# Kernel optimization log

Measured on AMD Instinct MI355X. Metric: run time of the kernel, lower is better.

Reference implementation:

```python
import jax, jax.numpy as jnp
import numpy as np

B, S, E = 4, 2048, 1024
H = 4
DH = E // H          # 256 head dim
DQ = E // 4          # 256 quaternion d_model
ALPHA = 1.5
EPS = 1e-10
FOCUS = 0.9
SEL = 2.0


def setup_inputs() -> dict:
    key = jax.random.key(0)
    ks = jax.random.split(key, 6)
    sc = 0.02
    return {
        "x": jax.random.normal(ks[0], (B, S, E), dtype=jnp.float32),
        "in_proj_w": jax.random.normal(ks[1], (3 * E, E), dtype=jnp.float32) * sc,
        "in_proj_b": jnp.zeros((3 * E,), dtype=jnp.float32),
        "out_w": jax.random.normal(ks[2], (E, E), dtype=jnp.float32) * sc,
        "out_b": jnp.zeros((E,), dtype=jnp.float32),
        "m_w1": jax.random.normal(ks[3], (E, E), dtype=jnp.float32) * sc,
        "m_b1": jnp.zeros((E,), dtype=jnp.float32),
        "m_w2": jax.random.normal(ks[4], (E, E), dtype=jnp.float32) * sc,
        "m_b2": jnp.zeros((E,), dtype=jnp.float32),
    }


def quaternion_multiply(q1, q2):
    # Hamilton product over last dim of size 4 (complex-valued components).
    w1, x1, y1, z1 = q1[..., 0], q1[..., 1], q1[..., 2], q1[..., 3]
    w2, x2, y2, z2 = q2[..., 0], q2[..., 1], q2[..., 2], q2[..., 3]
    return jnp.stack([
        w1 * w2 - x1 * x2 - y1 * y2 - z1 * z2,
        w1 * x2 + x1 * w2 + y1 * z2 - z1 * y2,
        w1 * y2 - x1 * z2 + y1 * w2 + z1 * x2,
        w1 * z2 + x1 * y2 - y1 * x2 + z1 * w2,
    ], axis=-1)


def _mha(x, in_proj_w, in_proj_b, out_w, out_b):
    # torch nn.MultiheadAttention self-attention, batch_first
    qkv = x @ in_proj_w.T + in_proj_b              # [B,S,3E]
    q, k, v = jnp.split(qkv, 3, axis=-1)
    q = q.reshape(B, S, H, DH)
    k = k.reshape(B, S, H, DH)
    v = v.reshape(B, S, H, DH)
    scores = jnp.einsum('bqhd,bkhd->bhqk', q, k) / jnp.sqrt(jnp.float32(DH))
    attn = jax.nn.softmax(scores, axis=-1)
    out = jnp.einsum('bhqk,bkhd->bqhd', attn, v).reshape(B, S, E)
    return out @ out_w.T + out_b


def _spectral_attention(signal):
    sq = signal.reshape(B, S, DQ, 4)
    sfft = jnp.fft.fft(sq, axis=-3)                 # complex64, FFT over seq
    kk = jnp.arange(S, dtype=jnp.float32)
    filt = jnp.exp(1j * ALPHA * jnp.arctan(jnp.log(kk + EPS)))  # [S] complex
    sf = sfft * filt[None, :, None, None]
    inter = quaternion_multiply(quaternion_multiply(sf, sf), sf)
    attended = jnp.fft.ifft(inter, axis=-3).real
    return attended.reshape(B, S, E)


def reference(x, in_proj_w, in_proj_b, out_w, out_b, m_w1, m_b1, m_w2, m_b2):
    nicotinic = _mha(x, in_proj_w, in_proj_b, out_w, out_b)
    h = jax.nn.gelu(x @ m_w1.T + m_b1, approximate=False)
    muscarinic = h @ m_w2.T + m_b2
    chol = FOCUS * nicotinic + (1.0 - FOCUS) * muscarinic
    attn_w = _spectral_attention(chol * SEL)
    return x * attn_w
```

## Files before the change

### kernel.cpp

```cpp
#include <hip/hip_runtime.h>
#include <cstdint>

typedef _Float16 f16;
typedef unsigned short u16;
typedef __attribute__((ext_vector_type(8))) _Float16 half8;
typedef __attribute__((ext_vector_type(2))) __fp16 fp16x2;
typedef __attribute__((ext_vector_type(4))) float f32x4;

#define MFMA_F16(a, b, c) __builtin_amdgcn_mfma_f32_16x16x32_f16(a, b, c, 0, 0, 0)

#define WAITVM8() asm volatile("s_waitcnt vmcnt(8)" ::: "memory")
#define WAITVM4() asm volatile("s_waitcnt vmcnt(4)" ::: "memory")
#define WAITVM0() asm volatile("s_waitcnt vmcnt(0)" ::: "memory")
#define BARRIER() do { asm volatile("" ::: "memory"); __builtin_amdgcn_s_barrier(); \
                       asm volatile("" ::: "memory"); } while (0)

__device__ inline void stage16(const void* g, void* l) {
#if defined(__has_builtin) && __has_builtin(__builtin_amdgcn_global_load_lds)
  __builtin_amdgcn_global_load_lds(
      (const __attribute__((address_space(1))) unsigned*)g,
      (__attribute__((address_space(3))) unsigned*)l, 16, 0, 0);
#else
  *(int4*)l = *(const int4*)g;
#endif
}

__device__ inline int pack_f16(float a, float b) {
#if defined(__has_builtin) && __has_builtin(__builtin_amdgcn_cvt_pkrtz)
  union { fp16x2 h; int i; } u;
  u.h = __builtin_amdgcn_cvt_pkrtz(a, b);
  return u.i;
#else
  union { f16 h[2]; int i; } u;
  u.h[0] = (f16)a; u.h[1] = (f16)b;
  return u.i;
#endif
}

__global__ __launch_bounds__(256)
void conv_all(const float* __restrict__ x, const float* __restrict__ wqkv,
              const float* __restrict__ w1, const float* __restrict__ wout,
              const float* __restrict__ w2, f16* __restrict__ dst) {
  int i = (blockIdx.x * 256 + threadIdx.x) * 8;
  const float* src; size_t dofs; float sc = 1.0f;
  if (i < 8388608)       { src = x + i;               dofs = i; }
  else if (i < 11534336) { src = wqkv + (i - 8388608); dofs = i; }
  else if (i < 12582912) { src = w1 + (i - 11534336);  dofs = i; }
  else if (i < 13631488) {
    int t = i - 12582912; int j = t >> 10, k = t & 1023;
    src = wout + t; dofs = 12582912 + (size_t)j * 2048 + k; sc = 1.8f;
  } else {
    int t = i - 13631488; int j = t >> 10, k = t & 1023;
    src = w2 + t; dofs = 12582912 + (size_t)j * 2048 + 1024 + k; sc = 0.2f;
  }
  float4 a = *(const float4*)src;
  float4 b = *(const float4*)(src + 4);
  half8 h;
  h[0] = (f16)(a.x * sc); h[1] = (f16)(a.y * sc); h[2] = (f16)(a.z * sc); h[3] = (f16)(a.w * sc);
  h[4] = (f16)(b.x * sc); h[5] = (f16)(b.y * sc); h[6] = (f16)(b.z * sc); h[7] = (f16)(b.w * sc);
  *(half8*)(dst + dofs) = h;
}

template<int EPI>
__global__ __launch_bounds__(256, 2)
void gemm_f16(const f16* __restrict__ A, const f16* __restrict__ W,
              const float* __restrict__ bias0, const float* __restrict__ bias1,
              void* __restrict__ out0, void* __restrict__ out1, int N, int K) {
  __shared__ __align__(16) f16 lds[2][16384];
  const int tid = threadIdx.x;
  const int lane = tid & 63, w = tid >> 6;
  const int g = lane >> 4, lm = lane & 15;
  const int wr = w >> 1, wc = w & 1;
  const int m0 = blockIdx.y * 128, n0 = blockIdx.x * 128;

  const f16* src[8];
#pragma unroll
  for (int j = 0; j < 8; ++j) {
    int u = j * 256 + tid;
    if (u < 1024) {
      int row = u >> 3, s = u & 7;
      src[j] = A + (size_t)(m0 + row) * K + ((s ^ (row & 7)) << 3);
    } else {
      int v = u - 1024;
      int row = v >> 3, s = v & 7;
      src[j] = W + (size_t)(n0 + row) * K + ((s ^ (row & 7)) << 3);
    }
  }

  f32x4 acc[4][4];
#pragma unroll
  for (int mt = 0; mt < 4; ++mt)
#pragma unroll
    for (int nt = 0; nt < 4; ++nt) acc[mt][nt] = (f32x4){0.f, 0.f, 0.f, 0.f};

#pragma unroll
  for (int j = 0; j < 8; ++j) stage16(src[j], &lds[0][(j * 256 + tid) * 8]);
  __syncthreads();

  const int KT = K >> 6;
#pragma unroll 1
  for (int t = 0; t < KT; ++t) {
    const f16* bufA = lds[t & 1];
    const f16* bufB = bufA + 8192;
    if (t + 1 < KT) {
#pragma unroll
      for (int j = 0; j < 8; ++j) {
        src[j] += 64;
        stage16(src[j], &lds[(t + 1) & 1][(j * 256 + tid) * 8]);
      }
      WAITVM8();
    } else {
      WAITVM0();
    }
    BARRIER();
#pragma unroll
    for (int ks = 0; ks < 2; ++ks) {
      half8 a[4], b[4];
#pragma unroll
      for (int mt = 0; mt < 4; ++mt) {
        int row = wr * 64 + mt * 16 + lm;
        a[mt] = *(const half8*)(bufA + row * 64 + (((ks * 4 + g) ^ (row & 7)) << 3));
      }
#pragma unroll
      for (int nt = 0; nt < 4; ++nt) {
        int row = wc * 64 + nt * 16 + lm;
        b[nt] = *(const half8*)(bufB + row * 64 + (((ks * 4 + g) ^ (row & 7)) << 3));
      }
#pragma unroll
      for (int mt = 0; mt < 4; ++mt)
#pragma unroll
        for (int nt = 0; nt < 4; ++nt)
          acc[mt][nt] = MFMA_F16(a[mt], b[nt], acc[mt][nt]);
    }
    BARRIER();
  }

  const int crow = m0 + wr * 64 + g * 4;
  const int ccol = n0 + wc * 64 + lm;
  if (EPI == 3) {
    if (n0 < 3072) {
      f16* qk = (f16*)out0;
#pragma unroll
      for (int nt = 0; nt < 4; ++nt) {
        float bb = bias0[ccol + nt * 16];
#pragma unroll
        for (int mt = 0; mt < 4; ++mt)
#pragma unroll
          for (int r = 0; r < 4; ++r)
            qk[(size_t)(crow + mt * 16 + r) * 3072 + ccol + nt * 16] =
                (f16)(acc[mt][nt][r] + bb);
      }
    } else {
      f16* cat = (f16*)out1;
      const int hc = ccol - 3072;
#pragma unroll
      for (int nt = 0; nt < 4; ++nt) {
        float bb = bias1[hc + nt * 16];
#pragma unroll
        for (int mt = 0; mt < 4; ++mt)
#pragma unroll
          for (int r = 0; r < 4; ++r) {
            float v = acc[mt][nt][r] + bb;
            v = 0.5f * v * (1.0f + erff(v * 0.70710678118654752f));
            cat[(size_t)(crow + mt * 16 + r) * 2048 + 1024 + hc + nt * 16] = (f16)v;
          }
      }
    }
  } else {
    float* ch = (float*)out0;
#pragma unroll
    for (int nt = 0; nt < 4; ++nt) {
      float bb = 1.8f * bias0[ccol + nt * 16] + 0.2f * bias1[ccol + nt * 16];
#pragma unroll
      for (int mt = 0; mt < 4; ++mt)
#pragma unroll
        for (int r = 0; r < 4; ++r)
          ch[(size_t)(crow + mt * 16 + r) * 1024 + ccol + nt * 16] =
              acc[mt][nt][r] + bb;
    }
  }
}

__global__ __launch_bounds__(256)
void vtrans(const f16* __restrict__ qkv, f16* __restrict__ Vt) {
  __shared__ unsigned vlds[64][65];
  const int tid = threadIdx.x;
  const int bh = blockIdx.x >> 5, st = blockIdx.x & 31;
  const int b = bh >> 2, h = bh & 3;
  const int s0 = st * 64;
  const u16* q16 = (const u16*)qkv;
  u16* v16 = (u16*)Vt;
#pragma unroll 1
  for (int dc = 0; dc < 4; ++dc) {
    __syncthreads();
#pragma unroll 1
    for (int i = 0; i < 16; ++i) {
      int idx = i * 256 + tid;
      int s = idx >> 6, dl = idx & 63;
      vlds[dl][s] = q16[(size_t)(b * 2048 + s0 + s) * 3072 + 2048 + h * 256 + dc * 64 + dl];
    }
    __syncthreads();
#pragma unroll 1
    for (int i = 0; i < 16; ++i) {
      int idx = i * 256 + tid;
      int dl = idx >> 6, s = idx & 63;
      v16[((size_t)bh * 256 + dc * 64 + dl) * 2048 + s0 + s] = (u16)vlds[dl][s];
    }
  }
}

__global__ __launch_bounds__(256, 2)
void flash_f16(const f16* __restrict__ qkv, const f16* __restrict__ Vt,
               f16* __restrict__ attn) {
  __shared__ __align__(16) f16 lds[32768];
  const int tid = threadIdx.x;
  const int lane = tid & 63, w = tid >> 6;
  const int g = lane >> 4, lm = lane & 15;
  const int raw = blockIdx.x;
  const int bh = (raw & 7) * 2 + (raw >> 8);
  const int qt = (raw >> 3) & 31;
  const int b = bh >> 2, h = bh & 3;
  const int q0 = qt * 64 + w * 16;
  const float SC = 0.09016844005555896f;

  half8 qf[8];
  {
    const f16* qp = qkv + (size_t)(b * 2048 + q0 + lm) * 3072 + h * 256 + g * 8;
#pragma unroll
    for (int c = 0; c < 8; ++c) qf[c] = *(const half8*)(qp + c * 32);
  }

  const f16* kbase = qkv + (size_t)b * 2048 * 3072 + 1024 + h * 256;
  const f16* vbase = Vt + (size_t)bh * 256 * 2048;
  int kofs[4], vofs[4];
#pragma unroll
  for (int j = 0; j < 4; ++j) {
    int u = j * 256 + tid;
    int kv = u >> 5, s = u & 31;
    kofs[j] = kv * 3072 + ((s ^ (kv & 7)) << 3);
    int d = u >> 2, sl = u & 3;
    vofs[j] = d * 2048 + ((sl ^ ((d >> 1) & 3)) << 3);
  }

  f32x4 o[16];
#pragma unroll
  for (int f = 0; f < 16; ++f) o[f] = (f32x4){0.f, 0.f, 0.f, 0.f};
  float m = -3e38f, l = 0.f;
  half8 paP = (half8){0, 0, 0, 0, 0, 0, 0, 0};

#pragma unroll
  for (int j = 0; j < 4; ++j) stage16(kbase + kofs[j], &lds[(j * 256 + tid) * 8]);

#pragma unroll 1
  for (int t = 0; t < 64; ++t) {
    const int cb_ = t & 1;
    if (t < 63) {
      const int kt = (t + 1) * 98304;
#pragma unroll
      for (int j = 0; j < 4; ++j)
        stage16(kbase + kofs[j] + kt, &lds[(cb_ ^ 1) * 8192 + (j * 256 + tid) * 8]);
    }
    {
      const int vt_ = t * 32;
#pragma unroll
      for (int j = 0; j < 4; ++j)
        stage16(vbase + vofs[j] + vt_, &lds[16384 + cb_ * 8192 + (j * 256 + tid) * 8]);
    }
    if (t < 63) { WAITVM8(); } else { WAITVM4(); }
    BARRIER();

    const f16* kb = &lds[cb_ * 8192];

    f32x4 s0 = {0.f, 0.f, 0.f, 0.f}, s1 = {0.f, 0.f, 0.f, 0.f};
    __builtin_amdgcn_s_setprio(1);
#pragma unroll
    for (int c = 0; c < 8; ++c) {
      int slot = ((c * 4 + g) ^ (lm & 7)) << 3;
      half8 b0 = *(const half8*)(kb + lm * 256 + slot);
      half8 b1 = *(const half8*)(kb + (16 + lm) * 256 + slot);
      s0 = MFMA_F16(b0, qf[c], s0);
      s1 = MFMA_F16(b1, qf[c], s1);
    }
    __builtin_amdgcn_s_setprio(0);

    if (t > 0) {
      const f16* vbp = &lds[16384 + (cb_ ^ 1) * 8192];
      __builtin_amdgcn_s_setprio(1);
#pragma unroll
      for (int f = 0; f < 16; ++f) {
        int d = f * 16 + lm;
        half8 bv = *(const half8*)(vbp + d * 32 + ((g ^ ((d >> 1) & 3)) << 3));
        o[f] = MFMA_F16(paP, bv, o[f]);
      }
      __builtin_amdgcn_s_setprio(0);
    }

    float a0[4], a1[4];
#pragma unroll
    for (int r = 0; r < 4; ++r) { a0[r] = s0[r] * SC; a1[r] = s1[r] * SC; }
    float mx = fmaxf(fmaxf(fmaxf(a0[0], a0[1]), fmaxf(a0[2], a0[3])),
                     fmaxf(fmaxf(a1[0], a1[1]), fmaxf(a1[2], a1[3])));
    mx = fmaxf(mx, __shfl_xor(mx, 16));
    mx = fmaxf(mx, __shfl_xor(mx, 32));

    if (!__all(mx <= m + 8.0f)) {
      float mn = fmaxf(m, mx);
      float corr = exp2f(m - mn);
      m = mn; l *= corr;
#pragma unroll
      for (int r = 0; r < 4; ++r) {
        float cr = __shfl(corr, ((lane >> 2) & 12) + r);
#pragma unroll
        for (int f = 0; f < 16; ++f) o[f][r] *= cr;
      }
    }

    float e0[4], e1[4], rs;
#pragma unroll
    for (int r = 0; r < 4; ++r) { e0[r] = exp2f(a0[r] - m); e1[r] = exp2f(a1[r] - m); }
    rs = ((e0[0] + e0[1]) + (e0[2] + e0[3])) + ((e1[0] + e1[1]) + (e1[2] + e1[3]));
    rs += __shfl_xor(rs, 16);
    rs += __shfl_xor(rs, 32);
    l += rs;

    int A01 = pack_f16(e0[0], e0[1]);
    int A23 = pack_f16(e0[2], e0[3]);
    int B01 = pack_f16(e1[0], e1[1]);
    int B23 = pack_f16(e1[2], e1[3]);
    const int s1l = ((lane & 16) << 1) + lm;
    const int s2l = s1l + 16;
    int t0a = __shfl(A01, s1l), t0b = __shfl(B01, s1l);
    int t1a = __shfl(A23, s1l), t1b = __shfl(B23, s1l);
    int t2a = __shfl(A01, s2l), t2b = __shfl(B01, s2l);
    int t3a = __shfl(A23, s2l), t3b = __shfl(B23, s2l);
    union { int i[4]; half8 h; } pau;
    const bool hi = lane >= 32;
    pau.i[0] = hi ? t0b : t0a;
    pau.i[1] = hi ? t1b : t1a;
    pau.i[2] = hi ? t2b : t2a;
    pau.i[3] = hi ? t3b : t3a;
    paP = pau.h;

    BARRIER();
  }

  WAITVM0();
  BARRIER();
  {
    const f16* vbp = &lds[16384 + 8192];
#pragma unroll
    for (int f = 0; f < 16; ++f) {
      int d = f * 16 + lm;
      half8 bv = *(const half8*)(vbp + d * 32 + ((g ^ ((d >> 1) & 3)) << 3));
      o[f] = MFMA_F16(paP, bv, o[f]);
    }
  }

  float inv[4];
#pragma unroll
  for (int r = 0; r < 4; ++r) inv[r] = 1.0f / __shfl(l, ((lane >> 2) & 12) + r);
#pragma unroll
  for (int f = 0; f < 16; ++f)
#pragma unroll
    for (int r = 0; r < 4; ++r)
      attn[(size_t)(b * 2048 + q0 + g * 4 + r) * 2048 + h * 256 + f * 16 + lm] =
          (f16)(o[f][r] * inv[r]);
}

__device__ inline float2 cmul(float2 a, float2 b) {
  return make_float2(a.x * b.x - a.y * b.y, a.x * b.y + a.y * b.x);
}
__device__ inline float2 cmulc(float2 a, float2 b) {
  return make_float2(a.x * b.x + a.y * b.y, a.y * b.x - a.x * b.y);
}
__device__ inline void qcube(float2& w, float2& x, float2& y, float2& z, float2 f) {
  w = cmul(w, f); x = cmul(x, f); y = cmul(y, f); z = cmul(z, f);
  float2 a2 = cmul(w, w);
  float2 sx = cmul(x, x), sy = cmul(y, y), sz = cmul(z, z);
  float2 s = make_float2(sx.x + sy.x + sz.x, sx.y + sy.y + sz.y);
  float2 t3 = make_float2(a2.x - 3.f * s.x, a2.y - 3.f * s.y);
  float2 cf = make_float2(3.f * a2.x - s.x, 3.f * a2.y - s.y);
  w = cmul(w, t3); x = cmul(cf, x); y = cmul(cf, y); z = cmul(cf, z);
}

__device__ inline int fftpos(int k) {
  int kp = k >> 1;
  return ((k & 1) << 10) | ((kp & 3) << 8) | ((kp & 12) << 4) | (kp & 48)
       | ((kp >> 4) & 12) | ((kp >> 8) & 3);
}

__global__ __launch_bounds__(256)
void spectral4(const float* __restrict__ chol, const float* __restrict__ xin,
               float* __restrict__ outp) {
  __shared__ __align__(16) float2 Z[2][2048];
  __shared__ float2 tw[1024];
  const int tid = threadIdx.x;
  const int b = blockIdx.x >> 8;
  const int qd = blockIdx.x & 255;
  const size_t c0 = (size_t)qd * 4;
  const float* cb = chol + (size_t)b * 2048 * 1024;

  for (int j = tid; j < 1024; j += 256) {
    float ang = -6.2831853071795864769f * (float)j * (1.0f / 2048.0f);
    float sv, cv; sincosf(ang, &sv, &cv);
    tw[j] = make_float2(cv, sv);
  }
  for (int s = tid; s < 2048; s += 256) {
    float4 v = *(const float4*)(cb + (size_t)s * 1024 + c0);
    Z[0][s] = make_float2(v.x, v.y);
    Z[1][s] = make_float2(v.z, v.w);
  }
  __syncthreads();

#pragma unroll 1
  for (int it = 0; it < 8; ++it) {
    int gg = it * 256 + tid;
    int c = gg >> 10, j = gg & 1023;
    float2 a = Z[c][j], bb = Z[c][j + 1024];
    Z[c][j] = make_float2(a.x + bb.x, a.y + bb.y);
    Z[c][j + 1024] = cmul(make_float2(a.x - bb.x, a.y - bb.y), tw[j]);
  }
  __syncthreads();

#pragma unroll 1
  for (int lq = 8; lq >= 0; lq -= 2) {
    const int Q = 1 << lq, st = 512 >> lq;
#pragma unroll 1
    for (int it = 0; it < 4; ++it) {
      int gg = it * 256 + tid;
      int c = gg >> 9, bf = gg & 511;
      int j = bf & (Q - 1);
      int base = ((bf >> lq) << (lq + 2)) | j;
      float2 a = Z[c][base], bq = Z[c][base + Q];
      float2 cc = Z[c][base + 2 * Q], d = Z[c][base + 3 * Q];
      float2 t0 = make_float2(a.x + cc.x, a.y + cc.y);
      float2 t1 = make_float2(a.x - cc.x, a.y - cc.y);
      float2 t2 = make_float2(bq.x + d.x, bq.y + d.y);
      float2 bd = make_float2(bq.x - d.x, bq.y - d.y);
      float2 t3 = make_float2(bd.y, -bd.x);
      float2 y0 = make_float2(t0.x + t2.x, t0.y + t2.y);
      float2 y1 = make_float2(t1.x + t3.x, t1.y + t3.y);
      float2 y2 = make_float2(t0.x - t2.x, t0.y - t2.y);
      float2 y3 = make_float2(t1.x - t3.x, t1.y - t3.y);
      int i3 = 3 * j * st;
      float sg = (i3 & 1024) ? -1.f : 1.f;
      i3 &= 1023;
      Z[c][base] = y0;
      Z[c][base + Q] = cmul(y1, tw[j * st]);
      Z[c][base + 2 * Q] = cmul(y2, tw[2 * j * st]);
      float2 r3 = cmul(y3, tw[i3]);
      Z[c][base + 3 * Q] = make_float2(r3.x * sg, r3.y * sg);
    }
    __syncthreads();
  }

#pragma unroll 1
  for (int it = 0; it < 4; ++it) {
    int jj = it * 256 + tid;
    int nrep = (jj == 0) ? 2 : 1;
#pragma unroll 1
    for (int rep = 0; rep < nrep; ++rep) {
      int k  = (jj == 0) ? (rep ? 1024 : 0) : jj;
      int kn = (jj == 0) ? k : 2048 - jj;
      int p  = fftpos(k);
      int pp = fftpos(kn);
      float2 z0p = Z[0][p], z0q = Z[0][pp];
      float2 z1p = Z[1][p], z1q = Z[1][pp];
      float2 wk = make_float2(0.5f * (z0p.x + z0q.x), 0.5f * (z0p.y - z0q.y));
      float2 xk = make_float2(0.5f * (z0p.y + z0q.y), 0.5f * (z0q.x - z0p.x));
      float2 yk = make_float2(0.5f * (z1p.x + z1q.x), 0.5f * (z1p.y - z1q.y));
      float2 zk = make_float2(0.5f * (z1p.y + z1q.y), 0.5f * (z1q.x - z1p.x));
      float2 wn = make_float2(0.5f * (z0q.x + z0p.x), 0.5f * (z0q.y - z0p.y));
      float2 xn = make_float2(0.5f * (z0q.y + z0p.y), 0.5f * (z0p.x - z0q.x));
      float2 yn = make_float2(0.5f * (z1q.x + z1p.x), 0.5f * (z1q.y - z1p.y));
      float2 zn = make_float2(0.5f * (z1q.y + z1p.y), 0.5f * (z1p.x - z1q.x));
      float sk, ck, sn, cn;
      sincosf(1.5f * atanf(logf((float)k + 1e-10f)), &sk, &ck);
      sincosf(1.5f * atanf(logf((float)kn + 1e-10f)), &sn, &cn);
      qcube(wk, xk, yk, zk, make_float2(ck, sk));
      qcube(wn, xn, yn, zn, make_float2(cn, sn));
      Z[0][p]  = make_float2(0.5f * (wk.x + wn.x) - 0.5f * (xk.y - xn.y),
                             0.5f * (wk.y - wn.y) + 0.5f * (xk.x + xn.x));
      Z[0][pp] = make_float2(0.5f * (wn.x + wk.x) - 0.5f * (xn.y - xk.y),
                             0.5f * (wn.y - wk.y) + 0.5f * (xn.x + xk.x));
      Z[1][p]  = make_float2(0.5f * (yk.x + yn.x) - 0.5f * (zk.y - zn.y),
                             0.5f * (yk.y - yn.y) + 0.5f * (zk.x + zn.x));
      Z[1][pp] = make_float2(0.5f * (yn.x + yk.x) - 0.5f * (zn.y - zk.y),
                             0.5f * (yn.y - yk.y) + 0.5f * (zn.x + zk.x));
    }
  }
  __syncthreads();

#pragma unroll 1
  for (int lq = 0; lq <= 8; lq += 2) {
    const int Q = 1 << lq, st = 512 >> lq;
#pragma unroll 1
    for (int it = 0; it < 4; ++it) {
      int gg = it * 256 + tid;
      int c = gg >> 9, bf = gg & 511;
      int j = bf & (Q - 1);
      int base = ((bf >> lq) << (lq + 2)) | j;
      float2 a = Z[c][base];
      float2 bq = cmulc(Z[c][base + Q], tw[j * st]);
      float2 cc = cmulc(Z[c][base + 2 * Q], tw[2 * j * st]);
      int i3 = 3 * j * st;
      float sg = (i3 & 1024) ? -1.f : 1.f;
      i3 &= 1023;
      float2 d = cmulc(Z[c][base + 3 * Q], tw[i3]);
      d = make_float2(d.x * sg, d.y * sg);
      float2 t0 = make_float2(a.x + cc.x, a.y + cc.y);
      float2 t1 = make_float2(a.x - cc.x, a.y - cc.y);
      float2 t2 = make_float2(bq.x + d.x, bq.y + d.y);
      float2 bd = make_float2(bq.x - d.x, bq.y - d.y);
      float2 t3 = make_float2(-bd.y, bd.x);
      Z[c][base]         = make_float2(t0.x + t2.x, t0.y + t2.y);
      Z[c][base + Q]     = make_float2(t1.x + t3.x, t1.y + t3.y);
      Z[c][base + 2 * Q] = make_float2(t0.x - t2.x, t0.y - t2.y);
      Z[c][base + 3 * Q] = make_float2(t1.x - t3.x, t1.y - t3.y);
    }
    __syncthreads();
  }

#pragma unroll 1
  for (int it = 0; it < 8; ++it) {
    int gg = it * 256 + tid;
    int c = gg >> 10, j = gg & 1023;
    float2 a = Z[c][j];
    float2 bw = cmulc(Z[c][j + 1024], tw[j]);
    Z[c][j] = make_float2(a.x + bw.x, a.y + bw.y);
    Z[c][j + 1024] = make_float2(a.x - bw.x, a.y - bw.y);
  }
  __syncthreads();

  const float* xb = xin + (size_t)b * 2048 * 1024;
  float* ob = outp + (size_t)b * 2048 * 1024;
  const float inv = 1.0f / 2048.0f;
  for (int s = tid; s < 2048; s += 256) {
    float4 xv = *(const float4*)(xb + (size_t)s * 1024 + c0);
    float2 r0 = Z[0][s], r1 = Z[1][s];
    float4 o;
    o.x = xv.x * r0.x * inv;
    o.y = xv.y * r0.y * inv;
    o.z = xv.z * r1.x * inv;
    o.w = xv.w * r1.y * inv;
    *(float4*)(ob + (size_t)s * 1024 + c0) = o;
  }
}

extern "C" void kernel_launch(void* const* d_in, const int* in_sizes, int n_in,
                              void* d_out, int out_size, void* d_ws, size_t ws_size,
                              hipStream_t stream) {
  const float* x    = (const float*)d_in[0];
  const float* wqkv = (const float*)d_in[1];
  const float* bqkv = (const float*)d_in[2];
  const float* wout = (const float*)d_in[3];
  const float* bout = (const float*)d_in[4];
  const float* w1   = (const float*)d_in[5];
  const float* b1   = (const float*)d_in[6];
  const float* w2   = (const float*)d_in[7];
  const float* b2   = (const float*)d_in[8];
  float* out = (float*)d_out;
  char* wsb = (char*)d_ws;
  const size_t MB = 1048576;

  f16*   xf    = (f16*)(wsb);
  f16*   wqf   = (f16*)(wsb + 16 * MB);
  f16*   wcat  = (f16*)(wsb + 24 * MB);
  f16*   qkvF  = (f16*)(wsb + 32 * MB);
  f16*   VtF   = (f16*)(wsb + 80 * MB);
  f16*   cat   = (f16*)(wsb + 96 * MB);
  float* chol  = (float*)(wsb + 128 * MB);

  conv_all<<<7168, 256, 0, stream>>>(x, wqkv, w1, wout, w2, xf);

  gemm_f16<3><<<dim3(32, 64), 256, 0, stream>>>(xf, wqf, bqkv, b1, qkvF, cat, 4096, 1024);
  vtrans<<<512, 256, 0, stream>>>(qkvF, VtF);
  flash_f16<<<512, 256, 0, stream>>>(qkvF, VtF, cat);
  gemm_f16<4><<<dim3(8, 64), 256, 0, stream>>>(cat, wcat, bout, b2, chol, nullptr, 1024, 2048);
  spectral4<<<1024, 256, 0, stream>>>(chol, x, out);
}
```

Measured before the change: 401.5 us.

## Fuse V transpose into QKV GEMM, enlarge flash blocks, store chol in fp16

The QKV GEMM epilogue now writes the V columns transposed through LDS directly into the Vt layout, which removes the separate vtrans kernel and one pass over V. Both GEMMs remap workgroup IDs in an XCD-aware way to improve L2 locality. The flash kernel moves to 512-thread blocks covering 128 queries, so each staged K/V tile is shared by twice as many queries and fewer loads are issued per thread. The chol intermediate is stored in fp16 rather than fp32, halving that write and the spectral kernel's read at the cost of precision before the cubic FFT step.

After: 360.6 us. -10.2%, faster.

```diff
diff --git a/kernel.cpp b/kernel.cpp
--- a/kernel.cpp
+++ b/kernel.cpp
@@ -4,6 +4,7 @@
 typedef _Float16 f16;
 typedef unsigned short u16;
 typedef __attribute__((ext_vector_type(8))) _Float16 half8;
+typedef __attribute__((ext_vector_type(4))) _Float16 half4;
 typedef __attribute__((ext_vector_type(2))) __fp16 fp16x2;
 typedef __attribute__((ext_vector_type(4))) float f32x4;
 
@@ -11,6 +12,7 @@
 
 #define WAITVM8() asm volatile("s_waitcnt vmcnt(8)" ::: "memory")
 #define WAITVM4() asm volatile("s_waitcnt vmcnt(4)" ::: "memory")
+#define WAITVM2() asm volatile("s_waitcnt vmcnt(2)" ::: "memory")
 #define WAITVM0() asm volatile("s_waitcnt vmcnt(0)" ::: "memory")
 #define BARRIER() do { asm volatile("" ::: "memory"); __builtin_amdgcn_s_barrier(); \
                        asm volatile("" ::: "memory"); } while (0)
@@ -65,13 +67,18 @@
 __global__ __launch_bounds__(256, 2)
 void gemm_f16(const f16* __restrict__ A, const f16* __restrict__ W,
               const float* __restrict__ bias0, const float* __restrict__ bias1,
-              void* __restrict__ out0, void* __restrict__ out1, int N, int K) {
+              void* __restrict__ out0, void* __restrict__ out1,
+              f16* __restrict__ Vt, int N, int K) {
   __shared__ __align__(16) f16 lds[2][16384];
   const int tid = threadIdx.x;
   const int lane = tid & 63, w = tid >> 6;
   const int g = lane >> 4, lm = lane & 15;
   const int wr = w >> 1, wc = w & 1;
-  const int m0 = blockIdx.y * 128, n0 = blockIdx.x * 128;
+  const int nwg = gridDim.x * gridDim.y;
+  const int flat = blockIdx.y * gridDim.x + blockIdx.x;
+  const int logical = (flat & 7) * (nwg >> 3) + (flat >> 3);
+  const int bx = logical % gridDim.x, by = logical / gridDim.x;
+  const int m0 = by * 128, n0 = bx * 128;
 
   const f16* src[8];
 #pragma unroll
@@ -138,7 +145,7 @@
   const int crow = m0 + wr * 64 + g * 4;
   const int ccol = n0 + wc * 64 + lm;
   if (EPI == 3) {
-    if (n0 < 3072) {
+    if (n0 < 2048) {
       f16* qk = (f16*)out0;
 #pragma unroll
       for (int nt = 0; nt < 4; ++nt) {
@@ -149,6 +156,32 @@
           for (int r = 0; r < 4; ++r)
             qk[(size_t)(crow + mt * 16 + r) * 3072 + ccol + nt * 16] =
                 (f16)(acc[mt][nt][r] + bb);
+      }
+    } else if (n0 < 3072) {
+      f16* ldsT = (f16*)lds;
+#pragma unroll
+      for (int nt = 0; nt < 4; ++nt) {
+        float bb = bias0[ccol + nt * 16];
+        int c = wc * 64 + nt * 16 + lm;
+#pragma unroll
+        for (int mt = 0; mt < 4; ++mt) {
+          int r = wr * 64 + mt * 16 + g * 4;
+#pragma unroll
+          for (int rr = 0; rr < 4; ++rr)
+            ldsT[c * 136 + r + rr] = (f16)(acc[mt][nt][rr] + bb);
+        }
+      }
+      BARRIER();
+      const int vbase0 = n0 - 2048;
+      const int b = m0 >> 11, srow = m0 & 2047;
+#pragma unroll
+      for (int it = 0; it < 8; ++it) {
+        int id = it * 256 + tid;
+        int c = id >> 4, rb = id & 15;
+        int vcol = vbase0 + c;
+        int h = vcol >> 8, d = vcol & 255;
+        half8 v = *(half8*)&ldsT[c * 136 + rb * 8];
+        *(half8*)&Vt[(((size_t)(b * 4 + h)) * 256 + d) * 2048 + srow + rb * 8] = v;
       }
     } else {
       f16* cat = (f16*)out1;
@@ -167,7 +200,7 @@
       }
     }
   } else {
-    float* ch = (float*)out0;
+    f16* ch = (f16*)out0;
 #pragma unroll
     for (int nt = 0; nt < 4; ++nt) {
       float bb = 1.8f * bias0[ccol + nt * 16] + 0.2f * bias1[ccol + nt * 16];
@@ -176,40 +209,12 @@
 #pragma unroll
         for (int r = 0; r < 4; ++r)
           ch[(size_t)(crow + mt * 16 + r) * 1024 + ccol + nt * 16] =
-              acc[mt][nt][r] + bb;
-    }
-  }
-}
-
-__global__ __launch_bounds__(256)
-void vtrans(const f16* __restrict__ qkv, f16* __restrict__ Vt) {
-  __shared__ unsigned vlds[64][65];
-  const int tid = threadIdx.x;
-  const int bh = blockIdx.x >> 5, st = blockIdx.x & 31;
-  const int b = bh >> 2, h = bh & 3;
-  const int s0 = st * 64;
-  const u16* q16 = (const u16*)qkv;
-  u16* v16 = (u16*)Vt;
-#pragma unroll 1
-  for (int dc = 0; dc < 4; ++dc) {
-    __syncthreads();
-#pragma unroll 1
-    for (int i = 0; i < 16; ++i) {
-      int idx = i * 256 + tid;
-      int s = idx >> 6, dl = idx & 63;
-      vlds[dl][s] = q16[(size_t)(b * 2048 + s0 + s) * 3072 + 2048 + h * 256 + dc * 64 + dl];
-    }
-    __syncthreads();
-#pragma unroll 1
-    for (int i = 0; i < 16; ++i) {
-      int idx = i * 256 + tid;
-      int dl = idx >> 6, s = idx & 63;
-      v16[((size_t)bh * 256 + dc * 64 + dl) * 2048 + s0 + s] = (u16)vlds[dl][s];
-    }
-  }
-}
-
-__global__ __launch_bounds__(256, 2)
+              (f16)(acc[mt][nt][r] + bb);
+    }
+  }
+}
+
+__global__ __launch_bounds__(512, 2)
 void flash_f16(const f16* __restrict__ qkv, const f16* __restrict__ Vt,
                f16* __restrict__ attn) {
   __shared__ __align__(16) f16 lds[32768];
@@ -217,10 +222,10 @@
   const int lane = tid & 63, w = tid >> 6;
   const int g = lane >> 4, lm = lane & 15;
   const int raw = blockIdx.x;
-  const int bh = (raw & 7) * 2 + (raw >> 8);
-  const int qt = (raw >> 3) & 31;
+  const int bh = (raw & 7) * 2 + (raw >> 7);
+  const int qt = (raw >> 3) & 15;
   const int b = bh >> 2, h = bh & 3;
-  const int q0 = qt * 64 + w * 16;
+  const int q0 = qt * 128 + w * 16;
   const float SC = 0.09016844005555896f;
 
   half8 qf[8];
@@ -232,10 +237,10 @@
 
   const f16* kbase = qkv + (size_t)b * 2048 * 3072 + 1024 + h * 256;
   const f16* vbase = Vt + (size_t)bh * 256 * 2048;
-  int kofs[4], vofs[4];
-#pragma unroll
-  for (int j = 0; j < 4; ++j) {
-    int u = j * 256 + tid;
+  int kofs[2], vofs[2];
+#pragma unroll
+  for (int j = 0; j < 2; ++j) {
+    int u = j * 512 + tid;
     int kv = u >> 5, s = u & 31;
     kofs[j] = kv * 3072 + ((s ^ (kv & 7)) << 3);
     int d = u >> 2, sl = u & 3;
@@ -249,7 +254,7 @@
   half8 paP = (half8){0, 0, 0, 0, 0, 0, 0, 0};
 
 #pragma unroll
-  for (int j = 0; j < 4; ++j) stage16(kbase + kofs[j], &lds[(j * 256 + tid) * 8]);
+  for (int j = 0; j < 2; ++j) stage16(kbase + kofs[j], &lds[(j * 512 + tid) * 8]);
 
 #pragma unroll 1
   for (int t = 0; t < 64; ++t) {
@@ -257,16 +262,16 @@
     if (t < 63) {
       const int kt = (t + 1) * 98304;
 #pragma unroll
-      for (int j = 0; j < 4; ++j)
-        stage16(kbase + kofs[j] + kt, &lds[(cb_ ^ 1) * 8192 + (j * 256 + tid) * 8]);
+      for (int j = 0; j < 2; ++j)
+        stage16(kbase + kofs[j] + kt, &lds[(cb_ ^ 1) * 8192 + (j * 512 + tid) * 8]);
     }
     {
       const int vt_ = t * 32;
 #pragma unroll
-      for (int j = 0; j < 4; ++j)
-        stage16(vbase + vofs[j] + vt_, &lds[16384 + cb_ * 8192 + (j * 256 + tid) * 8]);
-    }
-    if (t < 63) { WAITVM8(); } else { WAITVM4(); }
+      for (int j = 0; j < 2; ++j)
+        stage16(vbase + vofs[j] + vt_, &lds[16384 + cb_ * 8192 + (j * 512 + tid) * 8]);
+    }
+    if (t < 63) { WAITVM4(); } else { WAITVM2(); }
     BARRIER();
 
     const f16* kb = &lds[cb_ * 8192];
@@ -390,7 +395,7 @@
 }
 
 __global__ __launch_bounds__(256)
-void spectral4(const float* __restrict__ chol, const float* __restrict__ xin,
+void spectral4(const f16* __restrict__ chol, const float* __restrict__ xin,
                float* __restrict__ outp) {
   __shared__ __align__(16) float2 Z[2][2048];
   __shared__ float2 tw[1024];
@@ -398,7 +403,7 @@
   const int b = blockIdx.x >> 8;
   const int qd = blockIdx.x & 255;
   const size_t c0 = (size_t)qd * 4;
-  const float* cb = chol + (size_t)b * 2048 * 1024;
+  const f16* cb = chol + (size_t)b * 2048 * 1024;
 
   for (int j = tid; j < 1024; j += 256) {
     float ang = -6.2831853071795864769f * (float)j * (1.0f / 2048.0f);
@@ -406,9 +411,9 @@
     tw[j] = make_float2(cv, sv);
   }
   for (int s = tid; s < 2048; s += 256) {
-    float4 v = *(const float4*)(cb + (size_t)s * 1024 + c0);
-    Z[0][s] = make_float2(v.x, v.y);
-    Z[1][s] = make_float2(v.z, v.w);
+    half4 v = *(const half4*)(cb + (size_t)s * 1024 + c0);
+    Z[0][s] = make_float2((float)v[0], (float)v[1]);
+    Z[1][s] = make_float2((float)v[2], (float)v[3]);
   }
   __syncthreads();
 
@@ -569,13 +574,12 @@
   f16*   qkvF  = (f16*)(wsb + 32 * MB);
   f16*   VtF   = (f16*)(wsb + 80 * MB);
   f16*   cat   = (f16*)(wsb + 96 * MB);
-  float* chol  = (float*)(wsb + 128 * MB);
+  f16*   chol  = (f16*)(wsb + 128 * MB);
 
   conv_all<<<7168, 256, 0, stream>>>(x, wqkv, w1, wout, w2, xf);
 
-  gemm_f16<3><<<dim3(32, 64), 256, 0, stream>>>(xf, wqf, bqkv, b1, qkvF, cat, 4096, 1024);
-  vtrans<<<512, 256, 0, stream>>>(qkvF, VtF);
-  flash_f16<<<512, 256, 0, stream>>>(qkvF, VtF, cat);
-  gemm_f16<4><<<dim3(8, 64), 256, 0, stream>>>(cat, wcat, bout, b2, chol, nullptr, 1024, 2048);
+  gemm_f16<3><<<dim3(32, 64), 256, 0, stream>>>(xf, wqf, bqkv, b1, qkvF, cat, VtF, 4096, 1024);
+  flash_f16<<<256, 512, 0, stream>>>(qkvF, VtF, cat);
+  gemm_f16<4><<<dim3(8, 64), 256, 0, stream>>>(cat, wcat, bout, b2, chol, nullptr, nullptr, 1024, 2048);
   spectral4<<<1024, 256, 0, stream>>>(chol, x, out);
 }
```
